# Performance work log

Hardware: AMD Instinct MI355X
Metric: run time of the kernel (lower is better)

## Reference

```python
import jax, jax.numpy as jnp
import numpy as np
import math

D_MODEL = 1024
H = 16
D_K = D_MODEL // H
B = 4
S = 2048
NEG = -1e9


def setup_inputs() -> dict:
    key = jax.random.key(0)
    ks = jax.random.split(key, 11)
    scale = 1.0 / math.sqrt(D_MODEL)
    inp = {
        'q': jax.random.normal(ks[0], (B, S, D_MODEL), dtype=jnp.float32),
        'k': jax.random.normal(ks[1], (B, S, D_MODEL), dtype=jnp.float32),
        'v': jax.random.normal(ks[2], (B, S, D_MODEL), dtype=jnp.float32),
        'wq': jax.random.normal(ks[3], (D_MODEL, D_MODEL), dtype=jnp.float32) * scale,
        'bq': jnp.zeros((D_MODEL,), dtype=jnp.float32),
        'wk': jax.random.normal(ks[4], (D_MODEL, D_MODEL), dtype=jnp.float32) * scale,
        'bk': jnp.zeros((D_MODEL,), dtype=jnp.float32),
        'wv': jax.random.normal(ks[5], (D_MODEL, D_MODEL), dtype=jnp.float32) * scale,
        'bv': jnp.zeros((D_MODEL,), dtype=jnp.float32),
        'wo': jax.random.normal(ks[6], (D_MODEL, D_MODEL), dtype=jnp.float32) * scale,
        'bo': jnp.zeros((D_MODEL,), dtype=jnp.float32),
        # broadcastable causal mask [1, 1, S, S]; 0 = masked out
        'mask': jnp.tril(jnp.ones((S, S), dtype=jnp.int32))[None, None, :, :],
    }
    return inp


def reference(q, k, v, wq, bq, wk, bk, wv, bv, wo, bo, mask):
    # QKV projections: x @ W^T + b (nn.Linear convention)
    def split_heads(x):  # [B, S, D] -> [B, H, S, d_k]
        return x.reshape(B, S, H, D_K).transpose(0, 2, 1, 3)

    query = split_heads(q @ wq.T + bq)
    key_ = split_heads(k @ wk.T + bk)
    value = split_heads(v @ wv.T + bv)

    # scaled dot-product attention with mask; scores: [B, H, S, S]
    scores = jnp.einsum('bhqd,bhkd->bhqk', query, key_) / math.sqrt(D_K)
    scores = jnp.where(mask == 0, jnp.float32(NEG), scores)
    attn = jax.nn.softmax(scores, axis=-1)
    ctx = jnp.einsum('bhqk,bhkd->bhqd', attn, value)  # [B, H, S, d_k]

    # merge heads and output projection
    ctx = ctx.transpose(0, 2, 1, 3).reshape(B, S, D_MODEL)
    return ctx @ wo.T + bo
```

## Files before the change

### kernel.cpp

```cpp
#include <hip/hip_runtime.h>

#define DEVI __device__ __forceinline__

typedef __attribute__((ext_vector_type(8))) __bf16 bf16x8;
typedef __attribute__((ext_vector_type(4))) float f32x4;
typedef __attribute__((ext_vector_type(16))) float f32x16;
typedef __attribute__((ext_vector_type(4))) unsigned uint32x4;

DEVI __bf16 f2bf(float f) {
  unsigned u = __builtin_bit_cast(unsigned, f);
  unsigned r = u + 0x7fffu + ((u >> 16) & 1u);
  unsigned short h = (unsigned short)(r >> 16);
  return __builtin_bit_cast(__bf16, h);
}

DEVI unsigned cvt_pk_bf16(float lo, float hi) {
  unsigned r;
  asm("v_cvt_pk_bf16_f32 %0, %1, %2" : "=v"(r) : "v"(lo), "v"(hi));
  return r;
}

DEVI void load_lds16(const void* g, void* l) {
  __builtin_amdgcn_global_load_lds((__attribute__((address_space(1))) const void*)g,
                                   (__attribute__((address_space(3))) void*)l,
                                   16, 0, 0);
}

__global__ void convert_bf16(const float* __restrict__ in, __bf16* __restrict__ out, int n8) {
  int stride = gridDim.x * blockDim.x;
  for (int i = blockIdx.x * blockDim.x + threadIdx.x; i < n8; i += stride) {
    float4 a = ((const float4*)in)[i * 2];
    float4 b = ((const float4*)in)[i * 2 + 1];
    bf16x8 o;
    o[0] = f2bf(a.x); o[1] = f2bf(a.y); o[2] = f2bf(a.z); o[3] = f2bf(a.w);
    o[4] = f2bf(b.x); o[5] = f2bf(b.y); o[6] = f2bf(b.z); o[7] = f2bf(b.w);
    ((bf16x8*)out)[i] = o;
  }
}

template<int MODE>
__global__ __launch_bounds__(256, 2) void gemm_bt(
    const __bf16* __restrict__ A, const __bf16* __restrict__ W,
    const float* __restrict__ bias, void* __restrict__ outp)
{
  __shared__ __bf16 As[2][128 * 32];
  __shared__ __bf16 Bs[2][128 * 32];
  const int tid = threadIdx.x;
  const int lane = tid & 63;
  const int ln = lane & 15, g = lane >> 4;
  const int w = tid >> 6;
  const int wr = w >> 1, wc = w & 1;
  const int id = blockIdx.y * 64 + blockIdx.x;
  const int bx = 8 * (id & 7) + ((id >> 3) & 7);
  const int by = id >> 6;
  const int row0 = bx * 128, col0 = by * 128;

  f32x4 acc[4][4] = {};

  auto stage = [&](int buf, int k0) {
#pragma unroll
    for (int i = 0; i < 2; ++i) {
      int c = tid + 256 * i;
      int r = c >> 2, ko = (c & 3) * 8;
      load_lds16(&A[(size_t)(row0 + r) * 1024 + k0 + ko], &As[buf][c * 8]);
      load_lds16(&W[(size_t)(col0 + r) * 1024 + k0 + ko], &Bs[buf][c * 8]);
    }
  };

  stage(0, 0);
#pragma unroll 2
  for (int kt = 0; kt < 32; ++kt) {
    __syncthreads();
    if (kt + 1 < 32) stage((kt + 1) & 1, (kt + 1) * 32);
    const __bf16* as = As[kt & 1];
    const __bf16* bs = Bs[kt & 1];
    bf16x8 aF[4], bF[4];
#pragma unroll
    for (int mi = 0; mi < 4; ++mi)
      aF[mi] = *(const bf16x8*)&as[(wr * 64 + mi * 16 + ln) * 32 + g * 8];
#pragma unroll
    for (int ni = 0; ni < 4; ++ni)
      bF[ni] = *(const bf16x8*)&bs[(wc * 64 + ni * 16 + ln) * 32 + g * 8];
    __builtin_amdgcn_s_setprio(1);
#pragma unroll
    for (int mi = 0; mi < 4; ++mi)
#pragma unroll
      for (int ni = 0; ni < 4; ++ni)
        acc[mi][ni] = __builtin_amdgcn_mfma_f32_16x16x32_bf16(aF[mi], bF[ni], acc[mi][ni], 0, 0, 0);
    __builtin_amdgcn_s_setprio(0);
  }

#pragma unroll
  for (int ni = 0; ni < 4; ++ni) {
    int n = col0 + wc * 64 + ni * 16 + ln;
    float bv = bias[n];
#pragma unroll
    for (int mi = 0; mi < 4; ++mi) {
#pragma unroll
      for (int i = 0; i < 4; ++i) {
        int m = row0 + wr * 64 + mi * 16 + g * 4 + i;
        float val = acc[mi][ni][i] + bv;
        if (MODE == 2) {
          ((float*)outp)[(size_t)m * 1024 + n] = val;
        } else {
          int b = m >> 11, s = m & 2047, h = n >> 6, d = n & 63;
          size_t idx = (MODE == 0)
            ? ((size_t)((b * 16 + h) * 2048 + s) * 64 + d)
            : ((size_t)((b * 16 + h) * 64 + d) * 2048 + s);
          ((__bf16*)outp)[idx] = f2bf(val);
        }
      }
    }
  }
}

__global__ __launch_bounds__(256, 4) void attn_fwd(
    const __bf16* __restrict__ Qh, const __bf16* __restrict__ Kh,
    const __bf16* __restrict__ Vt, __bf16* __restrict__ Ctx)
{
  __shared__ __bf16 Ks[2][64 * 64];
  __shared__ __bf16 Vs[2][64 * 64];

  const int tid = threadIdx.x;
  const int lane = tid & 63;
  const int l31 = lane & 31, hl = lane >> 5;
  const int w = tid >> 6;
  const int bh = blockIdx.x;
  const int b = bh >> 4, h = bh & 15;
  const float CE = 0.18033688f;
  const float MC = 40.0f * CE;

  auto stageKV = [&](int buf, int t) {
    int kv0 = t * 64;
#pragma unroll
    for (int i = 0; i < 2; ++i) {
      int c = tid + 256 * i;
      int r = c >> 3, sl = c & 7;
      int so = 8 * (sl ^ (r & 7));
      load_lds16(&Kh[((size_t)bh * 2048 + kv0 + r) * 64 + so], &Ks[buf][c * 8]);
      load_lds16(&Vt[((size_t)bh * 64 + r) * 2048 + kv0 + so], &Vs[buf][c * 8]);
    }
  };

  auto strip = [&](int qb) {
    const int q0 = qb * 128;
    const int qw = q0 + w * 32;
    const int qglob = qw + l31;
    const int nt = 2 * qb + 2;

    bf16x8 qF[4];
#pragma unroll
    for (int ds = 0; ds < 4; ++ds)
      qF[ds] = *(const bf16x8*)&Qh[((size_t)bh * 2048 + qglob) * 64 + ds * 16 + hl * 8];

    f32x16 oT[2] = {};
    float lrun = 0.f;

    __syncthreads();
    stageKV(0, 0);
    for (int t = 0; t < nt; ++t) {
      __syncthreads();
      if (t + 1 < nt) stageKV((t + 1) & 1, t + 1);
      const int kv0 = t * 64;
      if (kv0 > qw + 31) continue;
      const __bf16* ksm = Ks[t & 1];
      const __bf16* vsm = Vs[t & 1];

      f32x16 sT[2] = {};
#pragma unroll
      for (int kblk = 0; kblk < 2; ++kblk) {
        bf16x8 aK[4];
        const int r = kblk * 32 + l31;
#pragma unroll
        for (int ds = 0; ds < 4; ++ds)
          aK[ds] = *(const bf16x8*)&ksm[r * 64 + ((ds * 16 + hl * 8) ^ ((r & 7) * 8))];
        __builtin_amdgcn_s_setprio(1);
#pragma unroll
        for (int ds = 0; ds < 4; ++ds)
          sT[kblk] = __builtin_amdgcn_mfma_f32_32x32x16_bf16(aK[ds], qF[ds], sT[kblk], 0, 0, 0);
        __builtin_amdgcn_s_setprio(0);
      }

      if (kv0 + 63 > qw) {
#pragma unroll
        for (int kblk = 0; kblk < 2; ++kblk)
#pragma unroll
          for (int r = 0; r < 16; ++r) {
            int kvg = kv0 + kblk * 32 + (r & 3) + 8 * (r >> 2) + 4 * hl;
            sT[kblk][r] = (kvg <= qglob) ? sT[kblk][r] : -3e38f;
          }
      }

      unsigned c0[8], c1[8];
      float ps0 = 0.f, ps1 = 0.f, ps2 = 0.f, ps3 = 0.f;
#pragma unroll
      for (int w2 = 0; w2 < 8; ++w2) {
        float p0 = exp2f(__builtin_fmaf(sT[0][2 * w2],     CE, -MC));
        float p1 = exp2f(__builtin_fmaf(sT[0][2 * w2 + 1], CE, -MC));
        float p2 = exp2f(__builtin_fmaf(sT[1][2 * w2],     CE, -MC));
        float p3 = exp2f(__builtin_fmaf(sT[1][2 * w2 + 1], CE, -MC));
        ps0 += p0; ps1 += p1; ps2 += p2; ps3 += p3;
        c0[w2] = cvt_pk_bf16(p0, p1);
        c1[w2] = cvt_pk_bf16(p2, p3);
      }
      lrun += (ps0 + ps1) + (ps2 + ps3);

      uint32x4 Wv[4];
#pragma unroll
      for (int kblk = 0; kblk < 2; ++kblk)
#pragma unroll
        for (int ksl = 0; ksl < 2; ++ksl)
#pragma unroll
          for (int al = 0; al < 2; ++al) {
            unsigned cp = kblk ? c1[4 * ksl + al]     : c0[4 * ksl + al];
            unsigned cq = kblk ? c1[4 * ksl + 2 + al] : c0[4 * ksl + 2 + al];
            unsigned cqx = __shfl_xor(cq, 32);
            unsigned cpx = __shfl_xor(cp, 32);
            Wv[kblk * 2 + ksl][al]     = hl ? cqx : cp;
            Wv[kblk * 2 + ksl][al + 2] = hl ? cq  : cpx;
          }

#pragma unroll
      for (int dblk = 0; dblk < 2; ++dblk) {
        bf16x8 aV[4];
        const int r = dblk * 32 + l31;
#pragma unroll
        for (int ks = 0; ks < 4; ++ks)
          aV[ks] = *(const bf16x8*)&vsm[r * 64 + ((ks * 16 + hl * 8) ^ ((r & 7) * 8))];
        __builtin_amdgcn_s_setprio(1);
#pragma unroll
        for (int ks = 0; ks < 4; ++ks)
          oT[dblk] = __builtin_amdgcn_mfma_f32_32x32x16_bf16(
              aV[ks], __builtin_bit_cast(bf16x8, Wv[ks]), oT[dblk], 0, 0, 0);
        __builtin_amdgcn_s_setprio(0);
      }
    }

    lrun += __shfl_xor(lrun, 32);
    const float inv = 1.0f / fmaxf(lrun, 1e-30f);
#pragma unroll
    for (int dblk = 0; dblk < 2; ++dblk)
#pragma unroll
      for (int rb = 0; rb < 4; ++rb) {
        unsigned u0 = cvt_pk_bf16(oT[dblk][4 * rb]     * inv, oT[dblk][4 * rb + 1] * inv);
        unsigned u1 = cvt_pk_bf16(oT[dblk][4 * rb + 2] * inv, oT[dblk][4 * rb + 3] * inv);
        int d = dblk * 32 + rb * 8 + 4 * hl;
        size_t idx = ((size_t)(b * 2048 + qglob)) * 1024 + h * 64 + d;
        *(uint2*)&Ctx[idx] = make_uint2(u0, u1);
      }
  };

  strip(15 - (int)blockIdx.y);
  strip((int)blockIdx.y);
}

extern "C" void kernel_launch(void* const* d_in, const int* in_sizes, int n_in,
                              void* d_out, int out_size, void* d_ws, size_t ws_size,
                              hipStream_t stream) {
  const float* q  = (const float*)d_in[0];
  const float* k  = (const float*)d_in[1];
  const float* v  = (const float*)d_in[2];
  const float* wq = (const float*)d_in[3];
  const float* bq = (const float*)d_in[4];
  const float* wk = (const float*)d_in[5];
  const float* bk = (const float*)d_in[6];
  const float* wv = (const float*)d_in[7];
  const float* bv = (const float*)d_in[8];
  const float* wo = (const float*)d_in[9];
  const float* bo = (const float*)d_in[10];
  float* out = (float*)d_out;
  char* ws = (char*)d_ws;

  const size_t MB = 1024 * 1024;
  __bf16* Wqb  = (__bf16*)(ws + 0 * MB);
  __bf16* Wkb  = (__bf16*)(ws + 2 * MB);
  __bf16* Wvb  = (__bf16*)(ws + 4 * MB);
  __bf16* Wob  = (__bf16*)(ws + 6 * MB);
  __bf16* Abuf = (__bf16*)(ws + 8 * MB);
  __bf16* Qh   = (__bf16*)(ws + 24 * MB);
  __bf16* Kh   = (__bf16*)(ws + 40 * MB);
  __bf16* Vt   = (__bf16*)(ws + 56 * MB);
  __bf16* Ctx  = Abuf;

  const int W8 = 1024 * 1024 / 8;
  const int X8 = 8192 * 1024 / 8;
  auto cgrid = [](int n8) { int nb = (n8 + 255) / 256; return dim3((unsigned)(nb < 2048 ? nb : 2048)); };

  convert_bf16<<<cgrid(W8), 256, 0, stream>>>(wq, Wqb, W8);
  convert_bf16<<<cgrid(W8), 256, 0, stream>>>(wk, Wkb, W8);
  convert_bf16<<<cgrid(W8), 256, 0, stream>>>(wv, Wvb, W8);
  convert_bf16<<<cgrid(W8), 256, 0, stream>>>(wo, Wob, W8);

  dim3 ggrid(64, 8);
  convert_bf16<<<cgrid(X8), 256, 0, stream>>>(q, Abuf, X8);
  gemm_bt<0><<<ggrid, 256, 0, stream>>>(Abuf, Wqb, bq, Qh);
  convert_bf16<<<cgrid(X8), 256, 0, stream>>>(k, Abuf, X8);
  gemm_bt<0><<<ggrid, 256, 0, stream>>>(Abuf, Wkb, bk, Kh);
  convert_bf16<<<cgrid(X8), 256, 0, stream>>>(v, Abuf, X8);
  gemm_bt<1><<<ggrid, 256, 0, stream>>>(Abuf, Wvb, bv, Vt);

  attn_fwd<<<dim3(64, 8), 256, 0, stream>>>(Qh, Kh, Vt, Ctx);
  gemm_bt<2><<<ggrid, 256, 0, stream>>>(Ctx, Wob, bo, out);
}
```

Before: 216.2 us.

## Split KV tiles across two warp groups in attention and merge partial outputs

Doubles the attention block to 512 threads. Two groups of four warps each take alternating 64-row KV tiles from a pair staged together, so each group covers half the KV loop for the same 128 query rows. At the end, group 1 writes its partial outputs and row sums to LDS and group 0 adds them before normalising. This merge works without rescaling only because the softmax uses a fixed max constant. The intent is more waves and better latency hiding per query strip, at the cost of twice the LDS buffers (64KB per block), extra barriers and a reduction step.

```diff
diff --git a/kernel.cpp b/kernel.cpp
--- a/kernel.cpp
+++ b/kernel.cpp
@@ -114,39 +114,40 @@
   }
 }
 
-__global__ __launch_bounds__(256, 4) void attn_fwd(
+__global__ __launch_bounds__(512, 4) void attn_fwd(
     const __bf16* __restrict__ Qh, const __bf16* __restrict__ Kh,
     const __bf16* __restrict__ Vt, __bf16* __restrict__ Ctx)
 {
-  __shared__ __bf16 Ks[2][64 * 64];
-  __shared__ __bf16 Vs[2][64 * 64];
+  __shared__ __bf16 KVs[8][64 * 64];
 
   const int tid = threadIdx.x;
   const int lane = tid & 63;
   const int l31 = lane & 31, hl = lane >> 5;
   const int w = tid >> 6;
+  const int wq3 = w & 3, p = w >> 2;
   const int bh = blockIdx.x;
   const int b = bh >> 4, h = bh & 15;
   const float CE = 0.18033688f;
   const float MC = 40.0f * CE;
 
-  auto stageKV = [&](int buf, int t) {
-    int kv0 = t * 64;
+  auto stagePair = [&](int tp) {
+    const int base = 2 * (tp & 1);
+    const int c = tid;
+    const int r = c >> 3, sl = c & 7;
+    const int so = 8 * (sl ^ (r & 7));
 #pragma unroll
     for (int i = 0; i < 2; ++i) {
-      int c = tid + 256 * i;
-      int r = c >> 3, sl = c & 7;
-      int so = 8 * (sl ^ (r & 7));
-      load_lds16(&Kh[((size_t)bh * 2048 + kv0 + r) * 64 + so], &Ks[buf][c * 8]);
-      load_lds16(&Vt[((size_t)bh * 64 + r) * 2048 + kv0 + so], &Vs[buf][c * 8]);
+      const int kv0 = (2 * tp + i) * 64, s = base + i;
+      load_lds16(&Kh[((size_t)bh * 2048 + kv0 + r) * 64 + so], &KVs[s][c * 8]);
+      load_lds16(&Vt[((size_t)bh * 64 + r) * 2048 + kv0 + so], &KVs[4 + s][c * 8]);
     }
   };
 
   auto strip = [&](int qb) {
     const int q0 = qb * 128;
-    const int qw = q0 + w * 32;
+    const int qw = q0 + wq3 * 32;
     const int qglob = qw + l31;
-    const int nt = 2 * qb + 2;
+    const int np = qb + 1;
 
     bf16x8 qF[4];
 #pragma unroll
@@ -157,14 +158,14 @@
     float lrun = 0.f;
 
     __syncthreads();
-    stageKV(0, 0);
-    for (int t = 0; t < nt; ++t) {
+    stagePair(0);
+    for (int tp = 0; tp < np; ++tp) {
       __syncthreads();
-      if (t + 1 < nt) stageKV((t + 1) & 1, t + 1);
-      const int kv0 = t * 64;
+      if (tp + 1 < np) stagePair(tp + 1);
+      const int kv0 = (2 * tp + p) * 64;
       if (kv0 > qw + 31) continue;
-      const __bf16* ksm = Ks[t & 1];
-      const __bf16* vsm = Vs[t & 1];
+      const __bf16* ksm = KVs[2 * (tp & 1) + p];
+      const __bf16* vsm = KVs[4 + 2 * (tp & 1) + p];
 
       f32x16 sT[2] = {};
 #pragma unroll
@@ -236,18 +237,42 @@
       }
     }
 
-    lrun += __shfl_xor(lrun, 32);
-    const float inv = 1.0f / fmaxf(lrun, 1e-30f);
-#pragma unroll
-    for (int dblk = 0; dblk < 2; ++dblk)
-#pragma unroll
-      for (int rb = 0; rb < 4; ++rb) {
-        unsigned u0 = cvt_pk_bf16(oT[dblk][4 * rb]     * inv, oT[dblk][4 * rb + 1] * inv);
-        unsigned u1 = cvt_pk_bf16(oT[dblk][4 * rb + 2] * inv, oT[dblk][4 * rb + 3] * inv);
-        int d = dblk * 32 + rb * 8 + 4 * hl;
-        size_t idx = ((size_t)(b * 2048 + qglob)) * 1024 + h * 64 + d;
-        *(uint2*)&Ctx[idx] = make_uint2(u0, u1);
-      }
+    __syncthreads();
+    float* ex = (float*)KVs + wq3 * 2176 + lane * 34;
+    if (p == 1) {
+      lrun += __shfl_xor(lrun, 32);
+#pragma unroll
+      for (int dblk = 0; dblk < 2; ++dblk)
+#pragma unroll
+        for (int rb = 0; rb < 8; ++rb)
+          *(float2*)(ex + dblk * 16 + rb * 2) =
+              make_float2(oT[dblk][2 * rb], oT[dblk][2 * rb + 1]);
+      ex[32] = lrun;
+    }
+    __syncthreads();
+    if (p == 0) {
+      lrun += __shfl_xor(lrun, 32);
+      lrun += ex[32];
+#pragma unroll
+      for (int dblk = 0; dblk < 2; ++dblk)
+#pragma unroll
+        for (int rb = 0; rb < 8; ++rb) {
+          float2 v = *(float2*)(ex + dblk * 16 + rb * 2);
+          oT[dblk][2 * rb]     += v.x;
+          oT[dblk][2 * rb + 1] += v.y;
+        }
+      const float inv = 1.0f / fmaxf(lrun, 1e-30f);
+#pragma unroll
+      for (int dblk = 0; dblk < 2; ++dblk)
+#pragma unroll
+        for (int rb = 0; rb < 4; ++rb) {
+          unsigned u0 = cvt_pk_bf16(oT[dblk][4 * rb]     * inv, oT[dblk][4 * rb + 1] * inv);
+          unsigned u1 = cvt_pk_bf16(oT[dblk][4 * rb + 2] * inv, oT[dblk][4 * rb + 3] * inv);
+          int d = dblk * 32 + rb * 8 + 4 * hl;
+          size_t idx = ((size_t)(b * 2048 + qglob)) * 1024 + h * 64 + d;
+          *(uint2*)&Ctx[idx] = make_uint2(u0, u1);
+        }
+    }
   };
 
   strip(15 - (int)blockIdx.y);
@@ -299,6 +324,6 @@
   convert_bf16<<<cgrid(X8), 256, 0, stream>>>(v, Abuf, X8);
   gemm_bt<1><<<ggrid, 256, 0, stream>>>(Abuf, Wvb, bv, Vt);
 
-  attn_fwd<<<dim3(64, 8), 256, 0, stream>>>(Qh, Kh, Vt, Ctx);
+  attn_fwd<<<dim3(64, 8), 512, 0, stream>>>(Qh, Kh, Vt, Ctx);
   gemm_bt<2><<<ggrid, 256, 0, stream>>>(Ctx, Wob, bo, out);
 }
```

Result: faster. 211.8 us (-2.0%).
